# Optimization experiments

Measured on AMD Instinct MI355X. Metric: run time of the kernel, lower is better.

The kernel has to match this reference:

```python
import jax, jax.numpy as jnp
import numpy as np

NUM_CLASSES = 20
MEM_SIZE = 512      # memory_bank_size
MAX_VIEWS = 512
TEMP = 0.1
MOMENTUM = 0.999
IGNORE_IDX = 255
AUX_IDX = 254
EPS = 1e-12


def _nearest_resize(gt, Ho, Wo):
    # torch F.interpolate(mode='nearest'): src = floor(dst * in/out)
    B, Hi, Wi = gt.shape
    ri = (jnp.arange(Ho) * Hi) // Ho
    ci = (jnp.arange(Wo) * Wi) // Wo
    return gt[:, ri][:, :, ci]


def _norm_flat(p):
    # L2-normalize over channels, then [B, C, H, W] -> [B, H*W, C]
    p = p / jnp.maximum(jnp.linalg.norm(p, axis=1, keepdims=True), EPS)
    B, C = p.shape[0], p.shape[1]
    return p.reshape(B, C, -1).transpose(0, 2, 1)


def setup_inputs() -> dict:
    key = jax.random.key(0)
    k1, k2, k3, k4, k5 = jax.random.split(key, 5)
    B, D, H, W = 4, 256, 128, 128
    Hg, Wg = 512, 512
    return {
        'main_proj': jax.random.normal(k1, (B, D, H, W), dtype=jnp.float32),
        'main_gt': jax.random.randint(k2, (B, Hg, Wg), 0, NUM_CLASSES).astype(jnp.int64),
        'aux_proj': jax.random.normal(k3, (B, D, H, W), dtype=jnp.float32),
        'aux_gt': jax.random.randint(k4, (B, Hg, Wg), 0, NUM_CLASSES).astype(jnp.int64),
        'memory_bank': jax.random.normal(k5, (NUM_CLASSES, MEM_SIZE, D), dtype=jnp.float32),
    }


def reference(main_proj, main_gt, aux_proj, aux_gt, memory_bank):
    C, M, D = memory_bank.shape
    B, _, H, W = main_proj.shape
    mg = _nearest_resize(main_gt, H, W)
    ag = _nearest_resize(aux_gt, aux_proj.shape[2], aux_proj.shape[3])

    embd = jnp.concatenate([_norm_flat(main_proj), _norm_flat(aux_proj)], axis=1)
    embd = embd.reshape(-1, D)                       # [N, D]
    label = jnp.concatenate([mg.reshape(B, -1), ag.reshape(B, -1)], axis=1).reshape(-1)

    valid = label != IGNORE_IDX
    label = jnp.where(label == AUX_IDX, C - 1, label)

    # per-class gather: stable argsort puts class-c pixels first (deterministic
    # stand-in for torch.randperm selection)
    masks = (label[None, :] == jnp.arange(C)[:, None]) & valid[None, :]   # [C, N]
    counts = masks.sum(axis=1)                                           # [C]
    order = jnp.argsort(~masks, axis=1, stable=True)[:, :M]              # [C, M]
    sel = embd[order]                                                    # [C, M, D]
    sel_valid = jnp.arange(M)[None, :] < counts[:, None]                 # [C, M]

    # momentum scatter-update to memory bank (no grad through features)
    upd = MOMENTUM * memory_bank + (1.0 - MOMENTUM) * jax.lax.stop_gradient(sel)
    upd = upd / jnp.maximum(jnp.linalg.norm(upd, axis=2, keepdims=True), EPS)
    bank = jnp.where(sel_valid[..., None], upd, memory_bank)             # [C, M, D]

    # anchors from current batch (with grad)
    V = min(MAX_VIEWS, M)
    anchors = sel[:, :V].reshape(C * V, D)
    a_valid = sel_valid[:, :V].reshape(-1)
    a_lbl = jnp.repeat(jnp.arange(C), V)

    # contrastive samples from updated bank (constant w.r.t. grad)
    contras = bank.reshape(C * M, D)
    c_valid = jnp.linalg.norm(bank, axis=2).reshape(-1) > 0
    c_lbl = jnp.repeat(jnp.arange(C), M)

    # InfoNCE with masked softmax over valid contrastive columns
    scores = (anchors @ contras.T) / TEMP                                # [A, K]
    scores = jnp.where(c_valid[None, :], scores, -1e9)
    logp = jax.nn.log_softmax(scores, axis=1)
    pos = ((a_lbl[:, None] == c_lbl[None, :]) & c_valid[None, :]).astype(scores.dtype)
    pos_sum = (pos * logp).sum(axis=1)
    pos_cnt = pos.sum(axis=1)
    va = (pos_cnt > 0) & a_valid
    mlpp = jnp.where(va, pos_sum / jnp.maximum(pos_cnt, 1.0), 0.0)
    loss = -mlpp.sum() / jnp.maximum(va.sum(), 1).astype(scores.dtype)
    return loss
```

## Files before the change

kernel.cpp:

```cpp
#include <hip/hip_runtime.h>
#include <cstdint>
#include <math.h>

#define NCLS  20
#define MSZ   512
#define DIM   256
#define HW    16384
#define NPIX  131072
#define AROWS 10240
#define TEMP_INV 10.0f
#define EXP2K 14.4269504088896f

typedef __attribute__((ext_vector_type(8))) short bf16x8;
typedef __attribute__((ext_vector_type(4))) float f32x4;

__device__ __forceinline__ short f2bf(float f) {
    unsigned u = __float_as_uint(f);
    unsigned r = (u + 0x7FFFu + ((u >> 16) & 1u)) >> 16;
    return (short)r;
}
__device__ __forceinline__ float bf2f(short s) {
    return __uint_as_float(((unsigned)(unsigned short)s) << 16);
}
__device__ __forceinline__ float fexp2(float x) {
    float r;
    asm volatile("v_exp_f32 %0, %1" : "=v"(r) : "v"(x));
    return r;
}
__device__ __forceinline__ void gld16(const void* g, void* l) {
    __builtin_amdgcn_global_load_lds(
        (const __attribute__((address_space(1))) unsigned int*)(uintptr_t)g,
        (__attribute__((address_space(3))) unsigned int*)(unsigned int)(uintptr_t)l,
        16, 0, 0);
}

#define ZREG_FLOATS 15488

__global__ __launch_bounds__(256) void k_hist(const int* __restrict__ mg,
                                              const int* __restrict__ ag,
                                              int* __restrict__ labels,
                                              int* __restrict__ hist,
                                              int* __restrict__ row2pix,
                                              float* __restrict__ zreg) {
    int chunk = blockIdx.x, t = threadIdx.x;
    int lane = t & 63;
    int gi = chunk * 256 + t;
    if (gi < ZREG_FLOATS) zreg[gi] = 0.0f;
    if (gi < AROWS) row2pix[gi] = -1;

    int n = gi;
    int b = n >> 15, r = n & 32767;
    const int* g = (r < HW) ? mg : ag;
    int p = (r < HW) ? r : (r - HW);
    int h = p >> 7, w = p & 127;
    int lab = g[(((size_t)b * 512) + (size_t)(h << 2)) * 512 + (size_t)(w << 2)];
    if (lab == 255) lab = -1;
    else if (lab == 254) lab = NCLS - 1;
    labels[n] = lab;

    __shared__ int cnt20[NCLS];
    if (t < NCLS) cnt20[t] = 0;
    __syncthreads();
#pragma unroll
    for (int c = 0; c < NCLS; ++c) {
        unsigned long long m = __ballot(lab == c);
        if (lane == 0 && m) atomicAdd(&cnt20[c], __popcll(m));
    }
    __syncthreads();
    if (t < NCLS) hist[t * 512 + chunk] = cnt20[t];
}

__global__ __launch_bounds__(256) void k_write(const int* __restrict__ labels,
                                               const int* __restrict__ hist,
                                               int* __restrict__ row2pix,
                                               int* __restrict__ counts) {
    int chunk = blockIdx.x, t = threadIdx.x;
    int lane = t & 63, wv = t >> 6;
    __shared__ int cbase[NCLS];
    __shared__ int wcnt2[4][NCLS];

#pragma unroll
    for (int cc = 0; cc < 5; ++cc) {
        int c = wv * 5 + cc;
        int s = 0;
        for (int j = lane; j < chunk; j += 64) s += hist[c * 512 + j];
#pragma unroll
        for (int o = 32; o > 0; o >>= 1) s += __shfl_down(s, o, 64);
        if (lane == 0) cbase[c] = s;
    }

    int n = chunk * 256 + t;
    int lab = labels[n];
    int myrank = 0;
#pragma unroll
    for (int c = 0; c < NCLS; ++c) {
        unsigned long long m = __ballot(lab == c);
        if (lane == 0) wcnt2[wv][c] = __popcll(m);
        if (lab == c) myrank = __popcll(m & ((1ull << lane) - 1ull));
    }
    __syncthreads();
    if (lab >= 0) {
        int base = cbase[lab] + myrank;
        for (int w = 0; w < wv; ++w) base += wcnt2[w][lab];
        if (base < MSZ) row2pix[lab * MSZ + base] = n;
    }
    if (chunk == 511 && t < NCLS)
        counts[t] = cbase[t] + wcnt2[0][t] + wcnt2[1][t] + wcnt2[2][t] + wcnt2[3][t];
}

__global__ __launch_bounds__(256) void k_nbc(const float* __restrict__ mainp,
                                             const float* __restrict__ auxp,
                                             const int* __restrict__ row2pix,
                                             const float* __restrict__ bank,
                                             const int* __restrict__ counts,
                                             short* __restrict__ anchorsB,
                                             short* __restrict__ contrasB,
                                             int* __restrict__ c_valid,
                                             float* __restrict__ S,
                                             int* __restrict__ pcnt) {
    int blk = blockIdx.x;
    int c = blk >> 5;
    int t = threadIdx.x, lane = t & 63, wv = t >> 6;
    int cc = counts[c];
    int base = blk * 16;
    float sacc[4] = {0.f, 0.f, 0.f, 0.f};
    int vcnt = 0;

#pragma unroll
    for (int it = 0; it < 4; ++it) {
        int a = base + it * 4 + wv;
        int m = a & 511;
        int n = row2pix[a];
        float x[4];
        if (n >= 0) {
            int b = n >> 15, r = n & 32767;
            const float* src = (r < HW) ? mainp : auxp;
            int p = (r < HW) ? r : (r - HW);
            const float* gp = src + (size_t)b * DIM * HW + p;
#pragma unroll
            for (int q = 0; q < 4; ++q)
                x[q] = gp[(size_t)(lane * 4 + q) * HW];
        } else {
            x[0] = x[1] = x[2] = x[3] = 0.0f;
        }
        float ss = x[0]*x[0] + x[1]*x[1] + x[2]*x[2] + x[3]*x[3];
#pragma unroll
        for (int o = 1; o < 64; o <<= 1) ss += __shfl_xor(ss, o, 64);
        float scale = 1.0f / fmaxf(sqrtf(ss), 1e-12f);
        float ax[4];
#pragma unroll
        for (int q = 0; q < 4; ++q) ax[q] = x[q] * scale;
        short4 oa;
        oa.x = f2bf(ax[0]); oa.y = f2bf(ax[1]); oa.z = f2bf(ax[2]); oa.w = f2bf(ax[3]);
        *(short4*)&anchorsB[(size_t)a * DIM + lane * 4] = oa;

        bool upd = m < cc;
        float4 bv = *(const float4*)&bank[(size_t)a * DIM + lane * 4];
        float u[4];
        u[0] = upd ? 0.999f * bv.x + 0.001f * ax[0] : bv.x;
        u[1] = upd ? 0.999f * bv.y + 0.001f * ax[1] : bv.y;
        u[2] = upd ? 0.999f * bv.z + 0.001f * ax[2] : bv.z;
        u[3] = upd ? 0.999f * bv.w + 0.001f * ax[3] : bv.w;
        float ss2 = u[0]*u[0] + u[1]*u[1] + u[2]*u[2] + u[3]*u[3];
#pragma unroll
        for (int o = 1; o < 64; o <<= 1) ss2 += __shfl_xor(ss2, o, 64);
        float nrm = sqrtf(ss2);
        float inv = 1.0f / fmaxf(nrm, 1e-12f);
        short oc[4];
        oc[0] = f2bf(upd ? u[0] * inv : bv.x);
        oc[1] = f2bf(upd ? u[1] * inv : bv.y);
        oc[2] = f2bf(upd ? u[2] * inv : bv.z);
        oc[3] = f2bf(upd ? u[3] * inv : bv.w);
        *(short4*)&contrasB[(size_t)a * DIM + lane * 4] = *(short4*)oc;
        bool valid = nrm > 0.0f;
        if (lane == 0) {
            c_valid[a] = valid ? 1 : 0;
            vcnt += valid ? 1 : 0;
        }
        if (valid) {
#pragma unroll
            for (int q = 0; q < 4; ++q) sacc[q] += bf2f(oc[q]);
        }
    }

    __shared__ float s4[4][DIM];
    __shared__ int pv[4];
#pragma unroll
    for (int q = 0; q < 4; ++q) s4[wv][lane * 4 + q] = sacc[q];
    if (lane == 0) pv[wv] = vcnt;
    __syncthreads();
    float s = s4[0][t] + s4[1][t] + s4[2][t] + s4[3][t];
    atomicAdd(&S[c * DIM + t], s);
    if (t == 0) atomicAdd(&pcnt[c], pv[0] + pv[1] + pv[2] + pv[3]);
}

__global__ __launch_bounds__(512, 4) void k_score(const short* __restrict__ A,
                                                  const short* __restrict__ Bc,
                                                  const int* __restrict__ c_valid,
                                                  float* __restrict__ row_sumexp) {
    __shared__ short As[128 * 64];
    __shared__ short Bs[256 * 64];
    const int t = threadIdx.x;
    const int lane = t & 63, wv = t >> 6;
    const int wr = wv & 1, wc = wv >> 1;
    const int qr = lane >> 4, qc = lane & 15;
    const int s7 = qc & 7;
    const int row0 = blockIdx.x * 128, col0 = blockIdx.y * 256;

    const int rl8 = t >> 3;
    const int sdat = (t & 7) ^ (rl8 & 7);
    const short* Ag = A  + (size_t)row0 * DIM;
    const short* Bg = Bc + (size_t)col0 * DIM;

    const int sl0 = ((0 + qr) ^ s7) * 8;
    const int sl1 = ((4 + qr) ^ s7) * 8;

    f32x4 acc[4][4] = {};

    auto stage = [&](int kt) {
#pragma unroll
        for (int r = 0; r < 2; ++r)
            gld16(Ag + (size_t)(r * 64 + rl8) * DIM + kt * 64 + sdat * 8,
                  &As[(r * 64 + wv * 8) * 64]);
#pragma unroll
        for (int r = 0; r < 4; ++r)
            gld16(Bg + (size_t)(r * 64 + rl8) * DIM + kt * 64 + sdat * 8,
                  &Bs[(r * 64 + wv * 8) * 64]);
    };

    stage(0);
    for (int kt = 0; kt < 4; ++kt) {
        asm volatile("s_waitcnt vmcnt(0)" ::: "memory");
        asm volatile("s_barrier" ::: "memory");

        bf16x8 a0[4], b0[4], a1[4], b1[4];
#pragma unroll
        for (int rt = 0; rt < 4; ++rt)
            a0[rt] = *(const bf16x8*)&As[(wr * 64 + rt * 16 + qc) * 64 + sl0];
#pragma unroll
        for (int ct = 0; ct < 4; ++ct)
            b0[ct] = *(const bf16x8*)&Bs[(wc * 64 + ct * 16 + qc) * 64 + sl0];
#pragma unroll
        for (int rt = 0; rt < 4; ++rt)
#pragma unroll
            for (int ct = 0; ct < 4; ++ct)
                acc[rt][ct] = __builtin_amdgcn_mfma_f32_16x16x32_bf16(a0[rt], b0[ct], acc[rt][ct], 0, 0, 0);
#pragma unroll
        for (int rt = 0; rt < 4; ++rt)
            a1[rt] = *(const bf16x8*)&As[(wr * 64 + rt * 16 + qc) * 64 + sl1];
#pragma unroll
        for (int ct = 0; ct < 4; ++ct)
            b1[ct] = *(const bf16x8*)&Bs[(wc * 64 + ct * 16 + qc) * 64 + sl1];

        asm volatile("s_waitcnt lgkmcnt(0)" ::: "memory");
        __builtin_amdgcn_sched_barrier(0);
        asm volatile("s_barrier" ::: "memory");
        if (kt < 3) stage(kt + 1);

#pragma unroll
        for (int rt = 0; rt < 4; ++rt)
#pragma unroll
            for (int ct = 0; ct < 4; ++ct)
                acc[rt][ct] = __builtin_amdgcn_mfma_f32_16x16x32_bf16(a1[rt], b1[ct], acc[rt][ct], 0, 0, 0);
    }

    float cm[4];
#pragma unroll
    for (int ct = 0; ct < 4; ++ct)
        cm[ct] = c_valid[col0 + wc * 64 + ct * 16 + qc] ? 1.0f : 0.0f;
#pragma unroll
    for (int rt = 0; rt < 4; ++rt)
#pragma unroll
        for (int r = 0; r < 4; ++r) {
            float e = cm[0] * fexp2(acc[rt][0][r] * EXP2K)
                    + cm[1] * fexp2(acc[rt][1][r] * EXP2K)
                    + cm[2] * fexp2(acc[rt][2][r] * EXP2K)
                    + cm[3] * fexp2(acc[rt][3][r] * EXP2K);
#pragma unroll
            for (int o = 1; o < 16; o <<= 1) e += __shfl_xor(e, o, 64);
            if (qc == 0)
                atomicAdd(&row_sumexp[row0 + wr * 64 + rt * 16 + qr * 4 + r], e);
        }
}

__global__ __launch_bounds__(256) void k_fin(const short* __restrict__ anchorsB,
                                             const float* __restrict__ S,
                                             const int* __restrict__ counts,
                                             const int* __restrict__ pcnt,
                                             const float* __restrict__ row_sumexp,
                                             float* __restrict__ facc,
                                             int* __restrict__ done_cnt,
                                             float* __restrict__ out) {
    int blk = blockIdx.x;
    int c = blk >> 5;
    int t = threadIdx.x, lane = t & 63, wv = t >> 6;
    int pc = pcnt[c], cc = counts[c];
    float lsum = 0.0f, vc = 0.0f;

    for (int it = 0; it < 4; ++it) {
        int a = blk * 16 + it * 4 + wv;
        short4 a4 = *(const short4*)&anchorsB[(size_t)a * DIM + lane * 4];
        float4 s4 = *(const float4*)&S[c * DIM + lane * 4];
        float dot = bf2f(a4.x) * s4.x + bf2f(a4.y) * s4.y
                  + bf2f(a4.z) * s4.z + bf2f(a4.w) * s4.w;
#pragma unroll
        for (int o = 1; o < 64; o <<= 1) dot += __shfl_xor(dot, o, 64);
        if (lane == 0 && (a & 511) < cc && pc > 0) {
            float lse = logf(row_sumexp[a]);
            lsum += (TEMP_INV * dot - (float)pc * lse) / (float)pc;
            vc += 1.0f;
        }
    }

    __shared__ float wls[4], wvc[4];
    if (lane == 0) { wls[wv] = lsum; wvc[wv] = vc; }
    __syncthreads();
    if (t == 0) {
        atomicAdd(&facc[0], wls[0] + wls[1] + wls[2] + wls[3]);
        atomicAdd(&facc[1], wvc[0] + wvc[1] + wvc[2] + wvc[3]);
        __threadfence();
        unsigned d = atomicAdd((unsigned*)done_cnt, 1u);
        if (d == 639u) {
            __threadfence();
            float L = atomicAdd(&facc[0], 0.0f);
            float V = atomicAdd(&facc[1], 0.0f);
            out[0] = -L / fmaxf(V, 1.0f);
        }
    }
}

extern "C" void kernel_launch(void* const* d_in, const int* in_sizes, int n_in,
                              void* d_out, int out_size, void* d_ws, size_t ws_size,
                              hipStream_t stream) {
    const float* main_proj = (const float*)d_in[0];
    const int*   main_gt   = (const int*)d_in[1];
    const float* aux_proj  = (const float*)d_in[2];
    const int*   aux_gt    = (const int*)d_in[3];
    const float* bank      = (const float*)d_in[4];
    float* out = (float*)d_out;

    char* ws = (char*)d_ws;
    int*   labels     = (int*)ws;
    int*   hist       = (int*)(ws + 524288);
    int*   row2pix    = (int*)(ws + 565248);
    int*   c_valid    = (int*)(ws + 1089536);
    float* zreg       = (float*)(ws + 1130496);
    float* row_sumexp = zreg;
    float* S          = zreg + 10240;
    int*   pcnt       = (int*)(zreg + 15360);
    float* facc       = zreg + 15380;
    int*   done_cnt   = (int*)(zreg + 15382);
    int*   counts     = (int*)(ws + 1192448);
    short* anchorsB   = (short*)(ws + 11678464);
    short* contrasB   = (short*)(ws + 16921344);

    k_hist<<<512, 256, 0, stream>>>(main_gt, aux_gt, labels, hist, row2pix, zreg);
    k_write<<<512, 256, 0, stream>>>(labels, hist, row2pix, counts);
    k_nbc<<<AROWS / 16, 256, 0, stream>>>(main_proj, aux_proj, row2pix, bank, counts,
                                          anchorsB, contrasB, c_valid, S, pcnt);
    dim3 grid(AROWS / 128, AROWS / 256);
    k_score<<<grid, 512, 0, stream>>>(anchorsB, contrasB, c_valid, row_sumexp);
    k_fin<<<AROWS / 16, 256, 0, stream>>>(anchorsB, S, counts, pcnt, row_sumexp,
                                          facc, done_cnt, out);
}
```

Baseline: 260.1 us.

## Fuse histogram/write kernels via grid barrier and fold finalize into score kernel

Merges the label histogram and row-write kernels into one kernel that uses a global atomic spin barrier, so labels no longer go through global memory and one launch is removed. The finalize kernel is folded into the score kernel: the last column-block of each row tile, detected with a per-row-tile atomic counter, computes that tile's loss contribution and the last tile writes the output. The cost is an extra memset launch for the barrier flag, and the barrier relies on all 512 blocks being co-resident, which risks a deadlock if that does not hold.

```diff
diff --git a/kernel.cpp b/kernel.cpp
--- a/kernel.cpp
+++ b/kernel.cpp
@@ -36,14 +36,15 @@
 
 #define ZREG_FLOATS 15488
 
-__global__ __launch_bounds__(256) void k_hist(const int* __restrict__ mg,
-                                              const int* __restrict__ ag,
-                                              int* __restrict__ labels,
-                                              int* __restrict__ hist,
-                                              int* __restrict__ row2pix,
-                                              float* __restrict__ zreg) {
+__global__ __launch_bounds__(256) void k_histwrite(const int* __restrict__ mg,
+                                                   const int* __restrict__ ag,
+                                                   int* __restrict__ hist,
+                                                   int* __restrict__ row2pix,
+                                                   int* __restrict__ counts,
+                                                   float* __restrict__ zreg,
+                                                   int* __restrict__ hflag) {
     int chunk = blockIdx.x, t = threadIdx.x;
-    int lane = t & 63;
+    int lane = t & 63, wv = t >> 6;
     int gi = chunk * 256 + t;
     if (gi < ZREG_FLOATS) zreg[gi] = 0.0f;
     if (gi < AROWS) row2pix[gi] = -1;
@@ -56,52 +57,46 @@
     int lab = g[(((size_t)b * 512) + (size_t)(h << 2)) * 512 + (size_t)(w << 2)];
     if (lab == 255) lab = -1;
     else if (lab == 254) lab = NCLS - 1;
-    labels[n] = lab;
 
     __shared__ int cnt20[NCLS];
+    __shared__ int cbase[NCLS];
+    __shared__ int wcnt2[4][NCLS];
     if (t < NCLS) cnt20[t] = 0;
     __syncthreads();
+    int myrank = 0;
 #pragma unroll
     for (int c = 0; c < NCLS; ++c) {
         unsigned long long m = __ballot(lab == c);
-        if (lane == 0 && m) atomicAdd(&cnt20[c], __popcll(m));
+        if (lane == 0) {
+            wcnt2[wv][c] = __popcll(m);
+            if (m) atomicAdd(&cnt20[c], __popcll(m));
+        }
+        if (lab == c) myrank = __popcll(m & ((1ull << lane) - 1ull));
     }
     __syncthreads();
     if (t < NCLS) hist[t * 512 + chunk] = cnt20[t];
-}
-
-__global__ __launch_bounds__(256) void k_write(const int* __restrict__ labels,
-                                               const int* __restrict__ hist,
-                                               int* __restrict__ row2pix,
-                                               int* __restrict__ counts) {
-    int chunk = blockIdx.x, t = threadIdx.x;
-    int lane = t & 63, wv = t >> 6;
-    __shared__ int cbase[NCLS];
-    __shared__ int wcnt2[4][NCLS];
-
-#pragma unroll
-    for (int cc = 0; cc < 5; ++cc) {
-        int c = wv * 5 + cc;
+    __syncthreads();
+    if (t == 0) {
+        __threadfence();
+        atomicAdd(hflag, 1);
+        while (atomicAdd(hflag, 0) < 512) __builtin_amdgcn_s_sleep(8);
+    }
+    __syncthreads();
+    __threadfence();
+
+#pragma unroll
+    for (int cc5 = 0; cc5 < 5; ++cc5) {
+        int c = wv * 5 + cc5;
         int s = 0;
         for (int j = lane; j < chunk; j += 64) s += hist[c * 512 + j];
 #pragma unroll
         for (int o = 32; o > 0; o >>= 1) s += __shfl_down(s, o, 64);
         if (lane == 0) cbase[c] = s;
     }
-
-    int n = chunk * 256 + t;
-    int lab = labels[n];
-    int myrank = 0;
-#pragma unroll
-    for (int c = 0; c < NCLS; ++c) {
-        unsigned long long m = __ballot(lab == c);
-        if (lane == 0) wcnt2[wv][c] = __popcll(m);
-        if (lab == c) myrank = __popcll(m & ((1ull << lane) - 1ull));
-    }
     __syncthreads();
     if (lab >= 0) {
         int base = cbase[lab] + myrank;
-        for (int w = 0; w < wv; ++w) base += wcnt2[w][lab];
+        for (int w2 = 0; w2 < wv; ++w2) base += wcnt2[w2][lab];
         if (base < MSZ) row2pix[lab * MSZ + base] = n;
     }
     if (chunk == 511 && t < NCLS)
@@ -197,7 +192,14 @@
 __global__ __launch_bounds__(512, 4) void k_score(const short* __restrict__ A,
                                                   const short* __restrict__ Bc,
                                                   const int* __restrict__ c_valid,
-                                                  float* __restrict__ row_sumexp) {
+                                                  float* __restrict__ row_sumexp,
+                                                  const float* __restrict__ S,
+                                                  const int* __restrict__ counts,
+                                                  const int* __restrict__ pcnt,
+                                                  float* __restrict__ facc,
+                                                  int* __restrict__ done_cnt,
+                                                  int* __restrict__ rb_cnt,
+                                                  float* __restrict__ out) {
     __shared__ short As[128 * 64];
     __shared__ short Bs[256 * 64];
     const int t = threadIdx.x;
@@ -281,46 +283,47 @@
             if (qc == 0)
                 atomicAdd(&row_sumexp[row0 + wr * 64 + rt * 16 + qr * 4 + r], e);
         }
-}
-
-__global__ __launch_bounds__(256) void k_fin(const short* __restrict__ anchorsB,
-                                             const float* __restrict__ S,
-                                             const int* __restrict__ counts,
-                                             const int* __restrict__ pcnt,
-                                             const float* __restrict__ row_sumexp,
-                                             float* __restrict__ facc,
-                                             int* __restrict__ done_cnt,
-                                             float* __restrict__ out) {
-    int blk = blockIdx.x;
-    int c = blk >> 5;
-    int t = threadIdx.x, lane = t & 63, wv = t >> 6;
-    int pc = pcnt[c], cc = counts[c];
-    float lsum = 0.0f, vc = 0.0f;
-
-    for (int it = 0; it < 4; ++it) {
-        int a = blk * 16 + it * 4 + wv;
-        short4 a4 = *(const short4*)&anchorsB[(size_t)a * DIM + lane * 4];
-        float4 s4 = *(const float4*)&S[c * DIM + lane * 4];
-        float dot = bf2f(a4.x) * s4.x + bf2f(a4.y) * s4.y
-                  + bf2f(a4.z) * s4.z + bf2f(a4.w) * s4.w;
+
+    __shared__ int fin_s;
+    __syncthreads();
+    if (t == 0) {
+        __threadfence();
+        unsigned cdone = atomicAdd((unsigned*)&rb_cnt[blockIdx.x], 1u);
+        fin_s = (cdone == 39u) ? 1 : 0;
+    }
+    __syncthreads();
+    if (!fin_s) return;
+    __threadfence();
+
+    const int c = row0 >> 9;
+    const int pc = pcnt[c], cc = counts[c];
+    float lsum = 0.0f, vcn = 0.0f;
+    for (int it = 0; it < 16; ++it) {
+        int a = row0 + wv * 16 + it;
+        short4 a4 = *(const short4*)&A[(size_t)a * DIM + lane * 4];
+        float4 sv = *(const float4*)&S[c * DIM + lane * 4];
+        float dot = bf2f(a4.x) * sv.x + bf2f(a4.y) * sv.y
+                  + bf2f(a4.z) * sv.z + bf2f(a4.w) * sv.w;
 #pragma unroll
         for (int o = 1; o < 64; o <<= 1) dot += __shfl_xor(dot, o, 64);
         if (lane == 0 && (a & 511) < cc && pc > 0) {
-            float lse = logf(row_sumexp[a]);
+            float lse = logf(atomicAdd(&row_sumexp[a], 0.0f));
             lsum += (TEMP_INV * dot - (float)pc * lse) / (float)pc;
-            vc += 1.0f;
-        }
-    }
-
-    __shared__ float wls[4], wvc[4];
-    if (lane == 0) { wls[wv] = lsum; wvc[wv] = vc; }
+            vcn += 1.0f;
+        }
+    }
+    __shared__ float wls[8], wvc[8];
+    if (lane == 0) { wls[wv] = lsum; wvc[wv] = vcn; }
     __syncthreads();
     if (t == 0) {
-        atomicAdd(&facc[0], wls[0] + wls[1] + wls[2] + wls[3]);
-        atomicAdd(&facc[1], wvc[0] + wvc[1] + wvc[2] + wvc[3]);
+        float L8 = 0.f, V8 = 0.f;
+#pragma unroll
+        for (int i2 = 0; i2 < 8; ++i2) { L8 += wls[i2]; V8 += wvc[i2]; }
+        atomicAdd(&facc[0], L8);
+        atomicAdd(&facc[1], V8);
         __threadfence();
         unsigned d = atomicAdd((unsigned*)done_cnt, 1u);
-        if (d == 639u) {
+        if (d == 79u) {
             __threadfence();
             float L = atomicAdd(&facc[0], 0.0f);
             float V = atomicAdd(&facc[1], 0.0f);
@@ -340,7 +343,6 @@
     float* out = (float*)d_out;
 
     char* ws = (char*)d_ws;
-    int*   labels     = (int*)ws;
     int*   hist       = (int*)(ws + 524288);
     int*   row2pix    = (int*)(ws + 565248);
     int*   c_valid    = (int*)(ws + 1089536);
@@ -350,16 +352,17 @@
     int*   pcnt       = (int*)(zreg + 15360);
     float* facc       = zreg + 15380;
     int*   done_cnt   = (int*)(zreg + 15382);
+    int*   rb_cnt     = (int*)(zreg + 15383);
     int*   counts     = (int*)(ws + 1192448);
+    int*   hflag      = (int*)(ws + 1192704);
     short* anchorsB   = (short*)(ws + 11678464);
     short* contrasB   = (short*)(ws + 16921344);
 
-    k_hist<<<512, 256, 0, stream>>>(main_gt, aux_gt, labels, hist, row2pix, zreg);
-    k_write<<<512, 256, 0, stream>>>(labels, hist, row2pix, counts);
+    hipMemsetAsync(hflag, 0, 4, stream);
+    k_histwrite<<<512, 256, 0, stream>>>(main_gt, aux_gt, hist, row2pix, counts, zreg, hflag);
     k_nbc<<<AROWS / 16, 256, 0, stream>>>(main_proj, aux_proj, row2pix, bank, counts,
                                           anchorsB, contrasB, c_valid, S, pcnt);
     dim3 grid(AROWS / 128, AROWS / 256);
-    k_score<<<grid, 512, 0, stream>>>(anchorsB, contrasB, c_valid, row_sumexp);
-    k_fin<<<AROWS / 16, 256, 0, stream>>>(anchorsB, S, counts, pcnt, row_sumexp,
-                                          facc, done_cnt, out);
-}
+    k_score<<<grid, 512, 0, stream>>>(anchorsB, contrasB, c_valid, row_sumexp,
+                                      S, counts, pcnt, facc, done_cnt, rb_cnt, out);
+}
```

Result: slower. 364.3 us (+40.1%).
